# Optimization experiments

Measured on AMD Instinct MI355X. Metric: run time of the kernel, lower is better.

The kernel has to match this reference:

```python
import jax, jax.numpy as jnp
import numpy as np

K = 5
NEG = -1e9
EPS = 1e-5


def _to_pix(f):
    # [B,C,H,W] -> [C,B,H,W] -> [C, B*H*W] -> [B*H*W, C]
    C = f.shape[1]
    return jnp.transpose(f, (1, 0, 2, 3)).reshape(C, -1).T


def _bn(x, g, b):
    # BatchNorm1d in training mode: biased batch statistics
    m = jnp.mean(x, axis=0)
    v = jnp.var(x, axis=0)
    return (x - m) * jax.lax.rsqrt(v + EPS) * g + b


def _transf(x, W1, b1, g1, be1, W2, b2, g2, be2):
    h = jax.nn.relu(_bn(x @ W1.T + b1, g1, be1))
    return jax.nn.relu(_bn(h @ W2.T + b2, g2, be2))


def reference(inp_cont, inp_style, peers_cont, peers_style,
              W1, b1, g1, be1, W2, b2, g2, be2, cw1, cb1, cw2, cb2):
    B, Cs, H, W_ = inp_style.shape
    xi = _to_pix(inp_cont)     # [N, C]
    xp = _to_pix(peers_cont)   # [M, C]
    sp = _to_pix(peers_style)  # [M, Cs]

    # pairwise euclidean distance [N, M]
    d2 = (jnp.sum(xi * xi, axis=1, keepdims=True)
          + jnp.sum(xp * xp, axis=1)[None, :]
          - 2.0 * xi @ xp.T)
    dist = jnp.sqrt(jnp.maximum(d2, 0.0))

    # kth smallest distance per row (top-k of negated distances)
    kth = -jax.lax.top_k(-dist, K)[0][:, K - 1:K]  # [N, 1]

    # additive attention scores: conv1d with kernel_size == feature length == dot product
    ti = _transf(xi, W1, b1, g1, be1, W2, b2, g2, be2)  # [N, C/4]
    tp = _transf(xp, W1, b1, g1, be1, W2, b2, g2, be2)  # [M, C/4]
    a1 = ti @ cw1 + cb1  # [N]
    a2 = tp @ cw2 + cb2  # [M]
    att = a1[:, None] + a2[None, :]  # [N, M]

    knn_filter = jnp.where(dist > kth, NEG, 0.0)
    att = jax.nn.softmax(jax.nn.softplus(att) + knn_filter, axis=1)

    out = att @ sp  # [N, Cs]
    fmap = jnp.transpose(out.T.reshape(Cs, B, H, W_), (1, 0, 2, 3))
    return jnp.concatenate([inp_cont, fmap], axis=1)


def setup_inputs() -> dict:
    key = jax.random.key(0)
    ks = jax.random.split(key, 12)
    C, Cs = 256, 256
    inp = {
        "inp_cont": jax.random.normal(ks[0], (1, C, 64, 64), jnp.float32),
        "inp_style": jax.random.normal(ks[1], (1, Cs, 64, 64), jnp.float32),
        "peers_cont": jax.random.normal(ks[2], (4, C, 64, 64), jnp.float32),
        "peers_style": jax.random.normal(ks[3], (4, Cs, 64, 64), jnp.float32),
        "W1": jax.random.normal(ks[4], (C // 2, C), jnp.float32) * 0.05,
        "b1": jnp.zeros((C // 2,), jnp.float32),
        "g1": jnp.ones((C // 2,), jnp.float32),
        "be1": jnp.zeros((C // 2,), jnp.float32),
        "W2": jax.random.normal(ks[5], (C // 4, C // 2), jnp.float32) * 0.08,
        "b2": jnp.zeros((C // 4,), jnp.float32),
        "g2": jnp.ones((C // 4,), jnp.float32),
        "be2": jnp.zeros((C // 4,), jnp.float32),
        "cw1": jax.random.normal(ks[6], (C // 4,), jnp.float32) * 0.1,
        "cb1": jnp.zeros((), jnp.float32),
        "cw2": jax.random.normal(ks[7], (C // 4,), jnp.float32) * 0.1,
        "cb2": jnp.zeros((), jnp.float32),
    }
    return inp
```

## Files before the change

kernel.cpp:

```cpp
#include <hip/hip_runtime.h>
#include <math.h>

#define NROWS 4096
#define MCOLS 16384
#define CDIM  256

typedef _Float16 half8 __attribute__((ext_vector_type(8)));
typedef float f32x4 __attribute__((ext_vector_type(4)));
typedef float f32x16 __attribute__((ext_vector_type(16)));

static __device__ __forceinline__ float softplusf(float x) {
    return fmaxf(x, 0.0f) + log1pf(expf(-fabsf(x)));
}

#define TOPK_UPDATE(BV, BI, WORST, WP, V, IDX)                                 \
    if ((V) < (WORST)) {                                                       \
        BV[WP] = (V); BI[WP] = (IDX);                                          \
        WORST = BV[0]; WP = 0;                                                 \
        _Pragma("unroll")                                                      \
        for (int _q = 1; _q < 8; ++_q)                                         \
            if (BV[_q] > WORST) { WORST = BV[_q]; WP = _q; }                   \
    }

#define TOPK_FAST(BV, BI, WORST, GATE, TAU, V, IDX)                            \
    if ((V) < (GATE)) {                                                        \
        const int _wp = __float_as_int(WORST) & 7;                             \
        BV[_wp] = __uint_as_float((__float_as_uint(V) & ~7u) | (unsigned)_wp); \
        BI[_wp] = (IDX);                                                       \
        const float _m0 = fmaxf(fmaxf(BV[0], BV[1]), fmaxf(BV[2], BV[3]));     \
        const float _m1 = fmaxf(fmaxf(BV[4], BV[5]), fmaxf(BV[6], BV[7]));     \
        WORST = fmaxf(_m0, _m1);                                               \
        GATE = fminf(TAU, WORST);                                              \
    }

__global__ __launch_bounds__(256)
void copy_kernel(const float4* __restrict__ src, float4* __restrict__ dst, int n4) {
    int i = blockIdx.x * blockDim.x + threadIdx.x;
    if (i < n4) dst[i] = src[i];
}

__global__ __launch_bounds__(256)
void norms_kernel(const float* __restrict__ xiT, const float* __restrict__ xpT,
                  float* __restrict__ normI, float* __restrict__ normP) {
    const int t = threadIdx.x;
    const int col = blockIdx.x * 64 + (t >> 2);
    const int sub = t & 3;
    const float* p;
    int base;
    if (col < MCOLS) { p = xpT; base = (col >> 12) * (CDIM * 4096) + (col & 4095); }
    else             { p = xiT; base = col - MCOLS; }
    float s = 0.0f;
#pragma unroll 8
    for (int k = 0; k < 64; ++k) {
        const float v = p[base + (sub * 64 + k) * 4096];
        s = fmaf(v, v, s);
    }
    s += __shfl_xor(s, 1);
    s += __shfl_xor(s, 2);
    if (sub == 0) {
        if (col < MCOLS) normP[col] = s;
        else             normI[col - MCOLS] = s;
    }
}

__global__ __launch_bounds__(256)
void convert_kernel(const float* __restrict__ src, uint4* __restrict__ dhi,
                    uint4* __restrict__ dlo, int ncols) {
    __shared__ float S[64][65];
    const int t = threadIdx.x;
    const int tilesPerRow = ncols >> 6;
    const int colbase = (blockIdx.x % tilesPerRow) << 6;
    const int ktbase  = (blockIdx.x / tilesPerRow) << 6;
    const int b = colbase >> 12;
    const int pixbase = colbase & 4095;
    const float* sp = src + (size_t)b * (CDIM * 4096) + (size_t)ktbase * 4096 + pixbase;

    for (int i = t; i < 4096; i += 256) {
        int kk = i >> 6, cc = i & 63;
        S[kk][cc] = sp[kk * 4096 + cc];
    }
    __syncthreads();

    const int l = t & 63;
#pragma unroll
    for (int s = 0; s < 2; ++s) {
        const int pid  = (t >> 6) + 4 * s;
        const int ct_l = pid & 1;
        const int kt_l = pid >> 1;
        const int c_l  = ct_l * 32 + (l & 31);
        const int k_l  = kt_l * 16 + ((l >> 5) << 3);
        half8 h, lo;
#pragma unroll
        for (int j = 0; j < 8; ++j) {
            float v = S[k_l + j][c_l];
            _Float16 hv = (_Float16)v;
            h[j]  = hv;
            lo[j] = (_Float16)(v - (float)hv);
        }
        const int ct_g = (colbase >> 5) + ct_l;
        const int kt_g = (ktbase >> 4) + kt_l;
        const size_t off = (size_t)(ct_g * 16 + kt_g) * 64 + l;
        dhi[off] = *reinterpret_cast<uint4*>(&h);
        dlo[off] = *reinterpret_cast<uint4*>(&lo);
    }
}

__global__ __launch_bounds__(256, 2)
void dist_topk_mfma(const uint4* __restrict__ xpBhi, const uint4* __restrict__ xpBlo,
                    const uint4* __restrict__ xiBhi, const uint4* __restrict__ xiBlo,
                    const float* __restrict__ normP,
                    float* __restrict__ candV, int* __restrict__ candI,
                    int nsplit) {
    __shared__ __align__(16) char Abuf[2][32768];
    __shared__ __align__(16) float nPl[2048];

    const int t = threadIdx.x;
    const int w = t >> 6;
    const int l = t & 63;
    int rt, cs;
    if (nsplit == 16) { cs = ((blockIdx.x & 7) << 1) | ((blockIdx.x >> 3) & 1); rt = blockIdx.x >> 4; }
    else              { cs = blockIdx.x & 7;                                    rt = blockIdx.x >> 3; }
    const int niter = (MCOLS / 32) / nsplit;
    const int span  = MCOLS / nsplit;
    const int colbase = cs * span;
    const int ncand = nsplit * 8;

    for (int i = t; i < span; i += 256) nPl[i] = 0.5f * normP[colbase + i];

    uint4 bh[16], bl[16];
    const int ctg = rt * 4 + w;
#pragma unroll
    for (int kt = 0; kt < 16; ++kt) {
        bh[kt] = xiBhi[(size_t)(ctg * 16 + kt) * 64 + l];
        bl[kt] = xiBlo[(size_t)(ctg * 16 + kt) * 64 + l];
    }

    float bv[8]; int bi[8];
#pragma unroll
    for (int j = 0; j < 8; ++j) {
        bv[j] = __uint_as_float((0x7f7ffff8u) | (unsigned)j);
        bi[j] = -1;
    }
    float worst = bv[7], tau = bv[7], gate = bv[7];

    const char* gb = (w >= 2) ? (const char*)xpBlo : (const char*)xpBhi;
    const char* srcBase = gb + (size_t)(cs * niter) * 16384 + (w & 1) * 8192 + l * 16;
    char* dbBase = &Abuf[0][(w >= 2 ? 16384 : 0) + (w & 1) * 8192];

    auto stage = [&](int it, int buf) {
        const char* src = srcBase + (size_t)it * 16384;
        char* db = dbBase + buf * 32768;
#pragma unroll
        for (int kt = 0; kt < 8; ++kt)
            __builtin_amdgcn_global_load_lds(
                (const __attribute__((address_space(1))) void*)(src + kt * 1024),
                (__attribute__((address_space(3))) void*)(db + kt * 1024),
                16, 0, 0);
    };

    stage(0, 0);
    asm volatile("s_waitcnt vmcnt(0)" ::: "memory");
    __builtin_amdgcn_s_barrier();

    for (int it = 0; it < niter; ++it) {
        if (it < niter - 1) {
            stage(it + 1, (it + 1) & 1);
            asm volatile("s_waitcnt vmcnt(8)" ::: "memory");
        } else {
            asm volatile("s_waitcnt vmcnt(0)" ::: "memory");
        }
        __builtin_amdgcn_s_barrier();
        __builtin_amdgcn_sched_barrier(0);

        const char* Ab = Abuf[it & 1];

        f32x16 a0, a1;
#pragma unroll
        for (int r = 0; r < 16; ++r) { a0[r] = 0.0f; a1[r] = 0.0f; }
        __builtin_amdgcn_s_setprio(1);
#pragma unroll
        for (int kt = 0; kt < 16; ++kt) {
            const half8 ah = *reinterpret_cast<const half8*>(Ab + kt * 1024 + l * 16);
            const half8 al = *reinterpret_cast<const half8*>(Ab + 16384 + kt * 1024 + l * 16);
            const half8 vh = *reinterpret_cast<const half8*>(&bh[kt]);
            const half8 vl = *reinterpret_cast<const half8*>(&bl[kt]);
            a0 = __builtin_amdgcn_mfma_f32_32x32x16_f16(ah, vh, a0, 0, 0, 0);
            a1 = __builtin_amdgcn_mfma_f32_32x32x16_f16(ah, vl, a1, 0, 0, 0);
            a0 = __builtin_amdgcn_mfma_f32_32x32x16_f16(al, vh, a0, 0, 0, 0);
        }
        __builtin_amdgcn_s_setprio(0);

        float dv[16];
        const int lq = (l >> 5) << 2;
#pragma unroll
        for (int rq = 0; rq < 4; ++rq) {
            const float4 np4 = *reinterpret_cast<const float4*>(&nPl[it * 32 + rq * 8 + lq]);
            const float npv[4] = {np4.x, np4.y, np4.z, np4.w};
#pragma unroll
            for (int j = 0; j < 4; ++j) {
                const int r = rq * 4 + j;
                dv[r] = npv[j] - (a0[r] + a1[r]);
            }
        }
        float mn = dv[0];
#pragma unroll
        for (int r = 1; r < 16; ++r) mn = fminf(mn, dv[r]);
        const int ib = colbase + it * 32 + lq;
        if (__any(mn < gate)) {
#pragma unroll
            for (int r = 0; r < 16; ++r) {
                const int cb = ib + (r & 3) + 8 * (r >> 2);
                TOPK_FAST(bv, bi, worst, gate, tau, dv[r], cb);
            }
        }

        {
            tau = fminf(worst, __shfl_xor(worst, 32));
            gate = fminf(tau, worst);
        }

        __builtin_amdgcn_s_barrier();
    }

    float* mVal = (float*)&Abuf[0][0];
    int*   mIdx = (int*)&Abuf[0][8192];

    __syncthreads();
#pragma unroll
    for (int j = 0; j < 8; ++j) { mVal[t * 8 + j] = bv[j]; mIdx[t * 8 + j] = bi[j]; }
    __syncthreads();
    if (t < 128) {
        const int t1 = ((t >> 5) << 6) + (t & 31);
        const int t2 = t1 + 32;
        float sv[8]; int si[8];
#pragma unroll
        for (int j = 0; j < 8; ++j) { sv[j] = 3.4e38f; si[j] = -1; }
        float wv = 3.4e38f; int wp = 0;
#pragma unroll
        for (int j = 0; j < 8; ++j) {
            const float v1 = mVal[t1 * 8 + j];
            TOPK_UPDATE(sv, si, wv, wp, v1, mIdx[t1 * 8 + j]);
            const float v2 = mVal[t2 * 8 + j];
            TOPK_UPDATE(sv, si, wv, wp, v2, mIdx[t2 * 8 + j]);
        }
        for (int a = 1; a < 8; ++a) {
            float v = sv[a]; int ii = si[a]; int b2 = a - 1;
            while (b2 >= 0 && sv[b2] > v) { sv[b2+1] = sv[b2]; si[b2+1] = si[b2]; --b2; }
            sv[b2+1] = v; si[b2+1] = ii;
        }
        const int row = rt * 128 + t;
#pragma unroll
        for (int j = 0; j < 8; ++j) {
            candV[row * ncand + cs * 8 + j] = sv[j];
            candI[row * ncand + cs * 8 + j] = si[j];
        }
    }
}

__global__ __launch_bounds__(256)
void gemm1_kernel(const float* __restrict__ Xp, const float* __restrict__ Xi,
                  const float* __restrict__ W, const float* __restrict__ bias,
                  float* __restrict__ outP, float* __restrict__ outI) {
    __shared__ __align__(16) float Wl[128][68];
    const int t = threadIdx.x;
    const bool isP = blockIdx.x < 512;
    const int bid  = isP ? blockIdx.x : blockIdx.x - 512;
    const float* X = isP ? Xp : Xi;
    const int rows = isP ? 16384 : 4096;
    float* outT = isP ? outP : outI;
    const int rowblk = bid >> 1;
    const int ch     = bid & 1;

    const int r   = rowblk * 64 + (t & 63);
    const int kgb = (t >> 6) * 16;

    float acc[16];
#pragma unroll
    for (int q = 0; q < 16; ++q) acc[q] = 0.0f;

    for (int half = 0; half < 2; ++half) {
        __syncthreads();
        for (int i = t; i < 128 * 64; i += 256) {
            int k = i >> 7, c = i & 127;
            Wl[c][k] = W[(ch * 64 + k) * 256 + half * 128 + c];
        }
        __syncthreads();
#pragma unroll 2
        for (int c = 0; c < 128; ++c) {
            const int cg = half * 128 + c;
            const float x = X[(r >> 12) * (CDIM * 4096) + cg * 4096 + (r & 4095)];
#pragma unroll
            for (int q = 0; q < 4; ++q) {
                const float4 wv = *reinterpret_cast<const float4*>(&Wl[c][kgb + 4 * q]);
                acc[4 * q + 0] = fmaf(x, wv.x, acc[4 * q + 0]);
                acc[4 * q + 1] = fmaf(x, wv.y, acc[4 * q + 1]);
                acc[4 * q + 2] = fmaf(x, wv.z, acc[4 * q + 2]);
                acc[4 * q + 3] = fmaf(x, wv.w, acc[4 * q + 3]);
            }
        }
    }
#pragma unroll
    for (int q = 0; q < 16; ++q) {
        const int k = ch * 64 + kgb + q;
        outT[k * rows + r] = acc[q] + bias[k];
    }
}

__global__ __launch_bounds__(256)
void gemm2_kernel(const float* __restrict__ Hp, const float* __restrict__ Hi,
                  const float* __restrict__ W, const float* __restrict__ bias,
                  const float* __restrict__ statsP, const float* __restrict__ statsI,
                  const float* __restrict__ g, const float* __restrict__ be,
                  float* __restrict__ outP, float* __restrict__ outI) {
    __shared__ __align__(16) float Wl[128][68];
    __shared__ float scL[128], shL[128];
    const int t = threadIdx.x;
    const bool isP = blockIdx.x < 256;
    const float* X = isP ? Hp : Hi;
    const float* stats = isP ? statsP : statsI;
    const float invDenom = isP ? (1.0f / 16384.0f) : (1.0f / 4096.0f);
    const int rows = isP ? 16384 : 4096;
    const int blk  = isP ? blockIdx.x : blockIdx.x - 256;
    float* outT = isP ? outP : outI;

    for (int i = t; i < 128 * 64; i += 256) {
        int k = i >> 7, c = i & 127;
        Wl[c][k] = W[k * 128 + c];
    }
    if (t < 128) {
        float mean = stats[t] * invDenom;
        float var  = stats[128 + t] * invDenom - mean * mean;
        float sc   = rsqrtf(var + 1e-5f) * g[t];
        scL[t] = sc;
        shL[t] = be[t] - mean * sc;
    }
    __syncthreads();

    const int r   = blk * 64 + (t & 63);
    const int chb = (t >> 6) * 16;

    float acc[16];
#pragma unroll
    for (int q = 0; q < 16; ++q) acc[q] = 0.0f;

#pragma unroll 2
    for (int c = 0; c < 128; ++c) {
        float x = X[c * rows + r];
        x = fmaxf(fmaf(x, scL[c], shL[c]), 0.0f);
#pragma unroll
        for (int q = 0; q < 4; ++q) {
            const float4 wv = *reinterpret_cast<const float4*>(&Wl[c][chb + 4 * q]);
            acc[4 * q + 0] = fmaf(x, wv.x, acc[4 * q + 0]);
            acc[4 * q + 1] = fmaf(x, wv.y, acc[4 * q + 1]);
            acc[4 * q + 2] = fmaf(x, wv.z, acc[4 * q + 2]);
            acc[4 * q + 3] = fmaf(x, wv.w, acc[4 * q + 3]);
        }
    }
#pragma unroll
    for (int q = 0; q < 16; ++q) {
        const int k = chb + q;
        outT[k * rows + r] = acc[q] + bias[k];
    }
}

__global__ __launch_bounds__(256)
void colstats2x_kernel(const float* __restrict__ Hp, const float* __restrict__ Hi,
                       int C, float* __restrict__ statsP, float* __restrict__ statsI) {
    __shared__ float rs[256], rq[256];
    const bool isP = blockIdx.x < (unsigned)C;
    const int c = isP ? blockIdx.x : blockIdx.x - C;
    const float* H = isP ? Hp : Hi;
    const int rows = isP ? 16384 : 4096;
    float* stats = isP ? statsP : statsI;
    const int t = threadIdx.x;
    float s = 0.0f, q = 0.0f;
    for (int r = t; r < rows; r += 256) {
        float v = H[c * rows + r];
        s += v;
        q = fmaf(v, v, q);
    }
    rs[t] = s; rq[t] = q;
    __syncthreads();
    for (int st = 128; st > 0; st >>= 1) {
        if (t < st) { rs[t] += rs[t + st]; rq[t] += rq[t + st]; }
        __syncthreads();
    }
    if (t == 0) { stats[c] = rs[0]; stats[C + c] = rq[0]; }
}

__global__ __launch_bounds__(256)
void a2x_kernel(const float* __restrict__ Hp, const float* __restrict__ Hi,
                const float* __restrict__ statsP, const float* __restrict__ statsI,
                const float* __restrict__ g, const float* __restrict__ be,
                const float* __restrict__ cwP, const float* __restrict__ cbP,
                const float* __restrict__ cwI, const float* __restrict__ cbI,
                float* __restrict__ aP, float* __restrict__ aI) {
    __shared__ float scL[64], shL[64], cwL[64];
    const bool isP = blockIdx.x < 64;
    const float* H = isP ? Hp : Hi;
    const float* stats = isP ? statsP : statsI;
    const float* cw = isP ? cwP : cwI;
    const float* cb = isP ? cbP : cbI;
    float* aout = isP ? aP : aI;
    const int rows = isP ? 16384 : 4096;
    const float invDenom = isP ? (1.0f / 16384.0f) : (1.0f / 4096.0f);
    const int blk = isP ? blockIdx.x : blockIdx.x - 64;
    const int t = threadIdx.x;
    if (t < 64) {
        float mean = stats[t] * invDenom;
        float var  = stats[64 + t] * invDenom - mean * mean;
        float sc   = rsqrtf(var + 1e-5f) * g[t];
        scL[t] = sc;
        shL[t] = be[t] - mean * sc;
        cwL[t] = cw[t];
    }
    __syncthreads();
    const int row = blk * 256 + t;
    if (row < rows) {
        float a = 0.0f;
        for (int c = 0; c < 64; ++c) {
            float v = H[c * rows + row];
            a += fmaxf(fmaf(v, scL[c], shL[c]), 0.0f) * cwL[c];
        }
        aout[row] = a + cb[0];
    }
}

__global__ __launch_bounds__(256)
void merge_kernel(const float* __restrict__ candV, const int* __restrict__ candI,
                  const float* __restrict__ a1, const float* __restrict__ a2,
                  float* __restrict__ w8, int* __restrict__ gidx, int ncand) {
    const int row = blockIdx.x * 256 + threadIdx.x;
    float sv[8]; int si[8];
#pragma unroll
    for (int j = 0; j < 8; ++j) { sv[j] = 3.4e38f; si[j] = 0; }
    float w2 = 3.4e38f; int wp = 0;
    for (int k = 0; k < ncand; ++k) {
        const float v = candV[row * ncand + k];
        TOPK_UPDATE(sv, si, w2, wp, v, candI[row * ncand + k]);
    }
    for (int a = 1; a < 8; ++a) {
        float v = sv[a]; int ii = si[a]; int b = a - 1;
        while (b >= 0 && sv[b] > v) { sv[b + 1] = sv[b]; si[b + 1] = si[b]; --b; }
        sv[b + 1] = v; si[b + 1] = ii;
    }
    const float kth = sv[4];
    int cnt = 5;
    while (cnt < 8 && sv[cnt] <= kth) ++cnt;

    const float arow = a1[row];
    float s[8], e[8];
    float mx = -1e30f;
#pragma unroll
    for (int j = 0; j < 8; ++j) s[j] = 0.0f;
    for (int j = 0; j < cnt; ++j) {
        s[j] = softplusf(arow + a2[si[j]]);
        mx = fmaxf(mx, s[j]);
    }
    float Z = 0.0f;
    for (int j = 0; j < 8; ++j) {
        e[j] = (j < cnt) ? expf(s[j] - mx) : 0.0f;
        Z += e[j];
    }
#pragma unroll
    for (int j = 0; j < 8; ++j) {
        const int ix = (j < cnt) ? si[j] : si[0];
        w8[row * 8 + j]   = e[j] / Z;
        gidx[row * 8 + j] = (ix >> 12) * (CDIM * 4096) + (ix & 4095);
    }
}

__global__ __launch_bounds__(256)
void gather_kernel(const float* __restrict__ w8, const int* __restrict__ gidx,
                   const float* __restrict__ PS, float* __restrict__ dout) {
    const int t = threadIdx.x;
    const int rtile = blockIdx.x >> 4;
    const int chunk = blockIdx.x & 15;
    const int row = rtile * 64 + (t & 63);
    const int c0  = chunk * 16 + (t >> 6) * 4;

    float w[8]; int ab[8];
#pragma unroll
    for (int j = 0; j < 8; ++j) { w[j] = w8[row * 8 + j]; ab[j] = gidx[row * 8 + j]; }

#pragma unroll
    for (int cc = 0; cc < 4; ++cc) {
        const int c = c0 + cc;
        float acc = 0.0f;
#pragma unroll
        for (int j = 0; j < 8; ++j) acc += w[j] * PS[ab[j] + c * 4096];
        dout[(CDIM + c) * 4096 + row] = acc;
    }
}

extern "C" void kernel_launch(void* const* d_in, const int* in_sizes, int n_in,
                              void* d_out, int out_size, void* d_ws, size_t ws_size,
                              hipStream_t stream) {
    const float* inp_cont    = (const float*)d_in[0];
    const float* peers_cont  = (const float*)d_in[2];
    const float* peers_style = (const float*)d_in[3];
    const float* W1  = (const float*)d_in[4];
    const float* b1  = (const float*)d_in[5];
    const float* g1  = (const float*)d_in[6];
    const float* be1 = (const float*)d_in[7];
    const float* W2  = (const float*)d_in[8];
    const float* b2  = (const float*)d_in[9];
    const float* g2  = (const float*)d_in[10];
    const float* be2 = (const float*)d_in[11];
    const float* cw1 = (const float*)d_in[12];
    const float* cb1 = (const float*)d_in[13];
    const float* cw2 = (const float*)d_in[14];
    const float* cb2 = (const float*)d_in[15];
    float* out = (float*)d_out;
    char*  wsb = (char*)d_ws;

    int nsplit;
    if      (ws_size >= (size_t)25400000) nsplit = 16;
    else if (ws_size >= (size_t)23300000) nsplit = 8;
    else return;
    const int ncand = nsplit * 8;
    const size_t candBytes = (size_t)NROWS * ncand * 4;

    uint4* xpBhi = (uint4*)(wsb + 0);
    uint4* xpBlo = (uint4*)(wsb + 8388608);
    uint4* xiBhi = (uint4*)(wsb + 16777216);
    uint4* xiBlo = (uint4*)(wsb + 18874368);
    float* normP = (float*)(wsb + 20971520);
    float* normI = (float*)(wsb + 21037056);
    float* candV = (float*)(wsb + 21053440);
    int*   candI = (int*)  (wsb + 21053440 + candBytes);
    char*  tail  = wsb + 21053440 + 2 * candBytes;
    float* a2    = (float*)(tail);
    float* a1    = (float*)(tail + 65536);
    float* s1p   = (float*)(tail + 81920);
    float* s1i   = (float*)(tail + 82944);
    float* s2p   = (float*)(tail + 83968);
    float* s2i   = (float*)(tail + 84480);
    float* H1Tp  = (float*)(wsb + 0);
    float* H2Tp  = (float*)(wsb + 8388608);
    float* H1Ti  = (float*)(wsb + 16777216);
    float* H2Ti  = (float*)(wsb + 18874368);
    float* w8    = (float*)(wsb + 19922944);
    int*   gidx  = (int*)  (wsb + 20054016);

    copy_kernel<<<1024, 256, 0, stream>>>((const float4*)inp_cont, (float4*)out, 262144);
    norms_kernel<<<320, 256, 0, stream>>>(inp_cont, peers_cont, normI, normP);
    convert_kernel<<<256, 256, 0, stream>>>(inp_cont, xiBhi, xiBlo, 4096);
    convert_kernel<<<1024, 256, 0, stream>>>(peers_cont, xpBhi, xpBlo, 16384);

    dist_topk_mfma<<<32 * nsplit, 256, 0, stream>>>(xpBhi, xpBlo, xiBhi, xiBlo,
                                                    normP, candV, candI, nsplit);

    gemm1_kernel<<<640, 256, 0, stream>>>(peers_cont, inp_cont, W1, b1, H1Tp, H1Ti);
    colstats2x_kernel<<<256, 256, 0, stream>>>(H1Tp, H1Ti, 128, s1p, s1i);
    gemm2_kernel<<<320, 256, 0, stream>>>(H1Tp, H1Ti, W2, b2, s1p, s1i, g1, be1, H2Tp, H2Ti);
    colstats2x_kernel<<<128, 256, 0, stream>>>(H2Tp, H2Ti, 64, s2p, s2i);
    a2x_kernel<<<80, 256, 0, stream>>>(H2Tp, H2Ti, s2p, s2i, g2, be2,
                                       cw2, cb2, cw1, cb1, a2, a1);

    merge_kernel<<<16, 256, 0, stream>>>(candV, candI, a1, a2, w8, gidx, ncand);
    gather_kernel<<<1024, 256, 0, stream>>>(w8, gidx, peers_style, out);
}
```

Baseline: 343.1 us.

## Process two query-row tiles per wave in distance/top-k kernel to reuse staged peer tiles

Each wave now holds two 32-row query tiles in registers (A and B) and runs MFMAs for both against every LDS-staged peer tile, doubling rows per block from 128 to 256 and halving the grid. This halves global-to-LDS traffic for peer data per query row and gives the MFMA pipe more independent accumulators. In exchange, register use roughly doubles, so launch bounds drop to one block per CU, lowering occupancy, and the final merge now uses all 256 threads over a larger LDS scratch.

```diff
diff --git a/kernel.cpp b/kernel.cpp
--- a/kernel.cpp
+++ b/kernel.cpp
@@ -105,7 +105,7 @@
     }
 }
 
-__global__ __launch_bounds__(256, 2)
+__global__ __launch_bounds__(256, 1)
 void dist_topk_mfma(const uint4* __restrict__ xpBhi, const uint4* __restrict__ xpBlo,
                     const uint4* __restrict__ xiBhi, const uint4* __restrict__ xiBlo,
                     const float* __restrict__ normP,
@@ -127,21 +127,26 @@
 
     for (int i = t; i < span; i += 256) nPl[i] = 0.5f * normP[colbase + i];
 
-    uint4 bh[16], bl[16];
-    const int ctg = rt * 4 + w;
+    uint4 bhA[16], blA[16], bhB[16], blB[16];
+    const int ctgA = rt * 8 + w;
+    const int ctgB = ctgA + 4;
 #pragma unroll
     for (int kt = 0; kt < 16; ++kt) {
-        bh[kt] = xiBhi[(size_t)(ctg * 16 + kt) * 64 + l];
-        bl[kt] = xiBlo[(size_t)(ctg * 16 + kt) * 64 + l];
-    }
-
-    float bv[8]; int bi[8];
+        bhA[kt] = xiBhi[(size_t)(ctgA * 16 + kt) * 64 + l];
+        blA[kt] = xiBlo[(size_t)(ctgA * 16 + kt) * 64 + l];
+        bhB[kt] = xiBhi[(size_t)(ctgB * 16 + kt) * 64 + l];
+        blB[kt] = xiBlo[(size_t)(ctgB * 16 + kt) * 64 + l];
+    }
+
+    float bvA[8], bvB[8]; int biA[8], biB[8];
 #pragma unroll
     for (int j = 0; j < 8; ++j) {
-        bv[j] = __uint_as_float((0x7f7ffff8u) | (unsigned)j);
-        bi[j] = -1;
-    }
-    float worst = bv[7], tau = bv[7], gate = bv[7];
+        bvA[j] = __uint_as_float((0x7f7ffff8u) | (unsigned)j);
+        bvB[j] = bvA[j];
+        biA[j] = -1; biB[j] = -1;
+    }
+    float worstA = bvA[7], tauA = bvA[7], gateA = bvA[7];
+    float worstB = bvB[7], tauB = bvB[7], gateB = bvB[7];
 
     const char* gb = (w >= 2) ? (const char*)xpBlo : (const char*)xpBhi;
     const char* srcBase = gb + (size_t)(cs * niter) * 16384 + (w & 1) * 8192 + l * 16;
@@ -174,24 +179,29 @@
 
         const char* Ab = Abuf[it & 1];
 
-        f32x16 a0, a1;
-#pragma unroll
-        for (int r = 0; r < 16; ++r) { a0[r] = 0.0f; a1[r] = 0.0f; }
+        f32x16 a0A, a1A, a0B, a1B;
+#pragma unroll
+        for (int r = 0; r < 16; ++r) { a0A[r] = 0.0f; a1A[r] = 0.0f; a0B[r] = 0.0f; a1B[r] = 0.0f; }
         __builtin_amdgcn_s_setprio(1);
 #pragma unroll
         for (int kt = 0; kt < 16; ++kt) {
             const half8 ah = *reinterpret_cast<const half8*>(Ab + kt * 1024 + l * 16);
             const half8 al = *reinterpret_cast<const half8*>(Ab + 16384 + kt * 1024 + l * 16);
-            const half8 vh = *reinterpret_cast<const half8*>(&bh[kt]);
-            const half8 vl = *reinterpret_cast<const half8*>(&bl[kt]);
-            a0 = __builtin_amdgcn_mfma_f32_32x32x16_f16(ah, vh, a0, 0, 0, 0);
-            a1 = __builtin_amdgcn_mfma_f32_32x32x16_f16(ah, vl, a1, 0, 0, 0);
-            a0 = __builtin_amdgcn_mfma_f32_32x32x16_f16(al, vh, a0, 0, 0, 0);
+            const half8 vhA = *reinterpret_cast<const half8*>(&bhA[kt]);
+            const half8 vlA = *reinterpret_cast<const half8*>(&blA[kt]);
+            const half8 vhB = *reinterpret_cast<const half8*>(&bhB[kt]);
+            const half8 vlB = *reinterpret_cast<const half8*>(&blB[kt]);
+            a0A = __builtin_amdgcn_mfma_f32_32x32x16_f16(ah, vhA, a0A, 0, 0, 0);
+            a0B = __builtin_amdgcn_mfma_f32_32x32x16_f16(ah, vhB, a0B, 0, 0, 0);
+            a1A = __builtin_amdgcn_mfma_f32_32x32x16_f16(ah, vlA, a1A, 0, 0, 0);
+            a1B = __builtin_amdgcn_mfma_f32_32x32x16_f16(ah, vlB, a1B, 0, 0, 0);
+            a0A = __builtin_amdgcn_mfma_f32_32x32x16_f16(al, vhA, a0A, 0, 0, 0);
+            a0B = __builtin_amdgcn_mfma_f32_32x32x16_f16(al, vhB, a0B, 0, 0, 0);
         }
         __builtin_amdgcn_s_setprio(0);
 
-        float dv[16];
         const int lq = (l >> 5) << 2;
+        float dvA[16], dvB[16];
 #pragma unroll
         for (int rq = 0; rq < 4; ++rq) {
             const float4 np4 = *reinterpret_cast<const float4*>(&nPl[it * 32 + rq * 8 + lq]);
@@ -199,38 +209,55 @@
 #pragma unroll
             for (int j = 0; j < 4; ++j) {
                 const int r = rq * 4 + j;
-                dv[r] = npv[j] - (a0[r] + a1[r]);
+                dvA[r] = npv[j] - (a0A[r] + a1A[r]);
+                dvB[r] = npv[j] - (a0B[r] + a1B[r]);
             }
         }
-        float mn = dv[0];
-#pragma unroll
-        for (int r = 1; r < 16; ++r) mn = fminf(mn, dv[r]);
+        float mnA = dvA[0], mnB = dvB[0];
+#pragma unroll
+        for (int r = 1; r < 16; ++r) { mnA = fminf(mnA, dvA[r]); mnB = fminf(mnB, dvB[r]); }
         const int ib = colbase + it * 32 + lq;
-        if (__any(mn < gate)) {
+        if (__any(mnA < gateA)) {
 #pragma unroll
             for (int r = 0; r < 16; ++r) {
                 const int cb = ib + (r & 3) + 8 * (r >> 2);
-                TOPK_FAST(bv, bi, worst, gate, tau, dv[r], cb);
+                TOPK_FAST(bvA, biA, worstA, gateA, tauA, dvA[r], cb);
             }
         }
+        if (__any(mnB < gateB)) {
+#pragma unroll
+            for (int r = 0; r < 16; ++r) {
+                const int cb = ib + (r & 3) + 8 * (r >> 2);
+                TOPK_FAST(bvB, biB, worstB, gateB, tauB, dvB[r], cb);
+            }
+        }
 
         {
-            tau = fminf(worst, __shfl_xor(worst, 32));
-            gate = fminf(tau, worst);
+            tauA = fminf(worstA, __shfl_xor(worstA, 32));
+            gateA = fminf(tauA, worstA);
+            tauB = fminf(worstB, __shfl_xor(worstB, 32));
+            gateB = fminf(tauB, worstB);
         }
 
         __builtin_amdgcn_s_barrier();
     }
 
     float* mVal = (float*)&Abuf[0][0];
-    int*   mIdx = (int*)&Abuf[0][8192];
+    int*   mIdx = (int*)&Abuf[0][16384];
 
     __syncthreads();
 #pragma unroll
-    for (int j = 0; j < 8; ++j) { mVal[t * 8 + j] = bv[j]; mIdx[t * 8 + j] = bi[j]; }
+    for (int j = 0; j < 8; ++j) {
+        mVal[t * 8 + j] = bvA[j];          mIdx[t * 8 + j] = biA[j];
+        mVal[2048 + t * 8 + j] = bvB[j];   mIdx[2048 + t * 8 + j] = biB[j];
+    }
     __syncthreads();
-    if (t < 128) {
-        const int t1 = ((t >> 5) << 6) + (t & 31);
+    {
+        const int g = t >> 5;
+        const int r32 = t & 31;
+        const int w_src = g & 3;
+        const int off = (g >> 2) * 2048;
+        const int t1 = w_src * 64 + r32;
         const int t2 = t1 + 32;
         float sv[8]; int si[8];
 #pragma unroll
@@ -238,17 +265,17 @@
         float wv = 3.4e38f; int wp = 0;
 #pragma unroll
         for (int j = 0; j < 8; ++j) {
-            const float v1 = mVal[t1 * 8 + j];
-            TOPK_UPDATE(sv, si, wv, wp, v1, mIdx[t1 * 8 + j]);
-            const float v2 = mVal[t2 * 8 + j];
-            TOPK_UPDATE(sv, si, wv, wp, v2, mIdx[t2 * 8 + j]);
+            const float v1 = mVal[off + t1 * 8 + j];
+            TOPK_UPDATE(sv, si, wv, wp, v1, mIdx[off + t1 * 8 + j]);
+            const float v2 = mVal[off + t2 * 8 + j];
+            TOPK_UPDATE(sv, si, wv, wp, v2, mIdx[off + t2 * 8 + j]);
         }
         for (int a = 1; a < 8; ++a) {
             float v = sv[a]; int ii = si[a]; int b2 = a - 1;
             while (b2 >= 0 && sv[b2] > v) { sv[b2+1] = sv[b2]; si[b2+1] = si[b2]; --b2; }
             sv[b2+1] = v; si[b2+1] = ii;
         }
-        const int row = rt * 128 + t;
+        const int row = rt * 256 + t;
 #pragma unroll
         for (int j = 0; j < 8; ++j) {
             candV[row * ncand + cs * 8 + j] = sv[j];
@@ -548,7 +575,7 @@
     convert_kernel<<<256, 256, 0, stream>>>(inp_cont, xiBhi, xiBlo, 4096);
     convert_kernel<<<1024, 256, 0, stream>>>(peers_cont, xpBhi, xpBlo, 16384);
 
-    dist_topk_mfma<<<32 * nsplit, 256, 0, stream>>>(xpBhi, xpBlo, xiBhi, xiBlo,
+    dist_topk_mfma<<<16 * nsplit, 256, 0, stream>>>(xpBhi, xpBlo, xiBhi, xiBlo,
                                                     normP, candV, candI, nsplit);
 
     gemm1_kernel<<<640, 256, 0, stream>>>(peers_cont, inp_cont, W1, b1, H1Tp, H1Ti);
```

Measured after the change: 388.8 us. +13.3%, slower.

## Transpose peer style to pixel-major layout for coalesced gather

Applied to the files above, without the earlier changes.

Adds a kernel that transposes peers_style from channel-major to pixel-major layout in workspace. The gather then reads contiguous float4 rows per selected neighbor and transposes the results through shared memory, so output writes stay coalesced. This replaces strided scattered reads with contiguous ones. In exchange it adds a full 16 MB read and write of peers_style on every call, and the gather grid shrinks to 128 blocks.

```diff
diff --git a/kernel.cpp b/kernel.cpp
--- a/kernel.cpp
+++ b/kernel.cpp
@@ -427,6 +427,27 @@
 }
 
 __global__ __launch_bounds__(256)
+void transpose_ps_kernel(const float* __restrict__ PS, float* __restrict__ PST) {
+    __shared__ float S[64][65];
+    const int t = threadIdx.x;
+    const int bid = blockIdx.x;
+    const int b  = bid >> 8;
+    const int cg = (bid >> 6) & 3;
+    const int pg = bid & 63;
+    const float* src = PS + (size_t)b * (CDIM * 4096) + (size_t)(cg * 64) * 4096 + pg * 64;
+    for (int i = t; i < 4096; i += 256) {
+        const int ch = i >> 6, px = i & 63;
+        S[ch][px] = src[ch * 4096 + px];
+    }
+    __syncthreads();
+    float* dst = PST + ((size_t)b * 4096 + pg * 64) * CDIM + cg * 64;
+    for (int i = t; i < 4096; i += 256) {
+        const int px = i >> 6, ch = i & 63;
+        dst[(size_t)px * CDIM + ch] = S[ch][px];
+    }
+}
+
+__global__ __launch_bounds__(256)
 void merge_kernel(const float* __restrict__ candV, const int* __restrict__ candI,
                   const float* __restrict__ a1, const float* __restrict__ a2,
                   float* __restrict__ w8, int* __restrict__ gidx, int ncand) {
@@ -464,32 +485,48 @@
     }
 #pragma unroll
     for (int j = 0; j < 8; ++j) {
-        const int ix = (j < cnt) ? si[j] : si[0];
         w8[row * 8 + j]   = e[j] / Z;
-        gidx[row * 8 + j] = (ix >> 12) * (CDIM * 4096) + (ix & 4095);
+        gidx[row * 8 + j] = (j < cnt) ? si[j] : si[0];
     }
 }
 
 __global__ __launch_bounds__(256)
 void gather_kernel(const float* __restrict__ w8, const int* __restrict__ gidx,
-                   const float* __restrict__ PS, float* __restrict__ dout) {
-    const int t = threadIdx.x;
-    const int rtile = blockIdx.x >> 4;
-    const int chunk = blockIdx.x & 15;
-    const int row = rtile * 64 + (t & 63);
-    const int c0  = chunk * 16 + (t >> 6) * 4;
-
-    float w[8]; int ab[8];
-#pragma unroll
-    for (int j = 0; j < 8; ++j) { w[j] = w8[row * 8 + j]; ab[j] = gidx[row * 8 + j]; }
-
-#pragma unroll
-    for (int cc = 0; cc < 4; ++cc) {
-        const int c = c0 + cc;
-        float acc = 0.0f;
-#pragma unroll
-        for (int j = 0; j < 8; ++j) acc += w[j] * PS[ab[j] + c * 4096];
-        dout[(CDIM + c) * 4096 + row] = acc;
+                   const float* __restrict__ PST, float* __restrict__ dout) {
+    __shared__ float T[32][261];
+    const int t = threadIdx.x;
+    const int w = t >> 6;
+    const int l = t & 63;
+    const int rowbase = blockIdx.x * 32;
+
+#pragma unroll
+    for (int rr = 0; rr < 8; ++rr) {
+        const int rloc = w * 8 + rr;
+        const int row = rowbase + rloc;
+        float ax = 0.0f, ay = 0.0f, az = 0.0f, aw = 0.0f;
+#pragma unroll
+        for (int j = 0; j < 8; ++j) {
+            const float wj = w8[row * 8 + j];
+            const int m = gidx[row * 8 + j];
+            const float4 v = *reinterpret_cast<const float4*>(&PST[(size_t)m * CDIM + l * 4]);
+            ax = fmaf(wj, v.x, ax);
+            ay = fmaf(wj, v.y, ay);
+            az = fmaf(wj, v.z, az);
+            aw = fmaf(wj, v.w, aw);
+        }
+        T[rloc][l * 4 + 0] = ax;
+        T[rloc][l * 4 + 1] = ay;
+        T[rloc][l * 4 + 2] = az;
+        T[rloc][l * 4 + 3] = aw;
+    }
+    __syncthreads();
+
+    const int rl = t & 31;
+    const int cb = t >> 5;
+#pragma unroll
+    for (int k = 0; k < 32; ++k) {
+        const int c = cb + 8 * k;
+        dout[(size_t)(CDIM + c) * 4096 + rowbase + rl] = T[rl][c];
     }
 }
 
@@ -542,6 +579,7 @@
     float* H2Ti  = (float*)(wsb + 18874368);
     float* w8    = (float*)(wsb + 19922944);
     int*   gidx  = (int*)  (wsb + 20054016);
+    float* PST   = (float*)(wsb + 0);
 
     copy_kernel<<<1024, 256, 0, stream>>>((const float4*)inp_cont, (float4*)out, 262144);
     norms_kernel<<<320, 256, 0, stream>>>(inp_cont, peers_cont, normI, normP);
@@ -558,6 +596,7 @@
     a2x_kernel<<<80, 256, 0, stream>>>(H2Tp, H2Ti, s2p, s2i, g2, be2,
                                        cw2, cb2, cw1, cb1, a2, a1);
 
+    transpose_ps_kernel<<<1024, 256, 0, stream>>>(peers_style, PST);
     merge_kernel<<<16, 256, 0, stream>>>(candV, candI, a1, a2, w8, gidx, ncand);
-    gather_kernel<<<1024, 256, 0, stream>>>(w8, gidx, peers_style, out);
-}
+    gather_kernel<<<128, 256, 0, stream>>>(w8, gidx, PST, out);
+}
```

Result: no change. 340.0 us (-0.9%).
